# Performance work log

Measured on AMD Instinct MI355X. Metric: run time of the kernel, lower is better.

Reference implementation:

```python
import jax, jax.numpy as jnp
import numpy as np

B, NB, TB = 16, 16, 256          # batch, num cache blocks, tokens per block
EMBED, NH, NKV, HD = 2048, 32, 8, 64  # embed dim, query heads, kv heads, head dim
LAST_OFFSET = 192                # valid length of the final cached block


def setup_inputs() -> dict:
    key = jax.random.key(0)
    ks = jax.random.split(key, 7)
    w = 0.02
    return {
        "x": jax.random.normal(ks[0], (B, 1, EMBED), jnp.float32),
        "blocks_k": jax.random.normal(ks[1], (NB, B, NKV, TB, HD), jnp.float32),
        "blocks_v": jax.random.normal(ks[2], (NB, B, NKV, TB, HD), jnp.float32),
        "Wq": jax.random.normal(ks[3], (EMBED, EMBED), jnp.float32) * w,
        "Wk": jax.random.normal(ks[4], (NKV * HD, EMBED), jnp.float32) * w,
        "Wv": jax.random.normal(ks[5], (NKV * HD, EMBED), jnp.float32) * w,
        "Wo": jax.random.normal(ks[6], (EMBED, EMBED), jnp.float32) * w,
        "last_offset": LAST_OFFSET,
    }


def reference(x, blocks_k, blocks_v, Wq, Wk, Wv, Wo, last_offset):
    # Decode step (T == 1) of GQA MultiHeadAttention with paged/blockwise KV cache.
    Bx, T, C = x.shape                      # T == 1
    nb, _, hkv, tb, hd = blocks_k.shape
    nh = C // hd
    g = nh // hkv                           # GQA group size
    scale = hd ** -0.5

    # Projections (nn.Linear with bias=False => x @ W.T)
    q = (x @ Wq.T).reshape(Bx, hkv, g, hd)          # (B, H_kv, g, D); T==1 folded
    k_cur = (x @ Wk.T).reshape(Bx, hkv, 1, hd)      # (B, H_kv, 1, D)
    v_cur = (x @ Wv.T).reshape(Bx, hkv, 1, hd)

    # Gather cached blocks into a contiguous view: (nb,B,Hkv,tb,D) -> (B,Hkv,nb*tb,D)
    Kc = jnp.transpose(blocks_k, (1, 2, 0, 3, 4)).reshape(Bx, hkv, nb * tb, hd)
    Vc = jnp.transpose(blocks_v, (1, 2, 0, 3, 4)).reshape(Bx, hkv, nb * tb, hd)
    K = jnp.concatenate([Kc, k_cur], axis=2)        # (B, H_kv, nb*tb+1, D)
    V = jnp.concatenate([Vc, v_cur], axis=2)

    # Valid positions: all full blocks, last cached block truncated to last_offset,
    # plus the current token. Equivalent to the streaming softmax over blocks.
    pos = jnp.arange(nb * tb)
    mask = jnp.concatenate([pos < (nb - 1) * tb + last_offset,
                            jnp.ones((1,), dtype=bool)])

    # GQA scores without materializing expanded KV heads
    scores = jnp.einsum('bhgd,bhkd->bhgk', q, K) * scale   # (B, H_kv, g, L)
    scores = jnp.where(mask, scores, jnp.finfo(scores.dtype).min)
    probs = jax.nn.softmax(scores, axis=-1)
    o = jnp.einsum('bhgk,bhkd->bhgd', probs, V)             # (B, H_kv, g, D)

    atten = o.reshape(Bx, 1, C)                              # heads -> channels
    out = atten @ Wo.T                                       # (B, 1, C)
    return out
```

## Files before the change

### kernel.cpp

```cpp
#include <hip/hip_runtime.h>
#include <cstdint>
#include <cstddef>

#define BATCH 16
#define NBLK 16
#define TB 256
#define EMBED 2048
#define NKV 8
#define GQ 4
#define HD 64
#define NQROWS 3072
#define QSCALE 0.18033688011112042f

#define OFF_PARTMS 49152
#define OFF_PARTO  65536
#define OFF_ATTEN  589824

__device__ __forceinline__ float dot4(float4 a, float4 b) {
  return a.x * b.x + a.y * b.y + a.z * b.z + a.w * b.w;
}

template <int CTRL>
__device__ __forceinline__ float dpp_add(float x) {
  return x + __int_as_float(
                 __builtin_amdgcn_mov_dpp(__float_as_int(x), CTRL, 0xF, 0xF, true));
}
__device__ __forceinline__ float red16(float x) {
  x = dpp_add<0xB1>(x);
  x = dpp_add<0x4E>(x);
  x = dpp_add<0x124>(x);
  x = dpp_add<0x128>(x);
  return x;
}

#define PROJ_RPB 4
__global__ __launch_bounds__(256) void proj_kernel(
    const float* __restrict__ x, const float* __restrict__ Wq,
    const float* __restrict__ Wk, const float* __restrict__ Wv,
    float* __restrict__ proj) {
  int tid = threadIdx.x;
  int bb = tid & 15, kc = tid >> 4;
  int row0 = blockIdx.x * PROJ_RPB;
  const float* xp = x + (size_t)bb * EMBED + kc * 128;
  const float* wr[PROJ_RPB];
#pragma unroll
  for (int r = 0; r < PROJ_RPB; ++r) {
    int row = row0 + r;
    wr[r] = (row < 2048 ? Wq + (size_t)row * EMBED
             : row < 2560 ? Wk + (size_t)(row - 2048) * EMBED
                          : Wv + (size_t)(row - 2560) * EMBED) + kc * 128;
  }
  float a[PROJ_RPB] = {0.f, 0.f, 0.f, 0.f};
#pragma unroll
  for (int k = 0; k < 128; k += 8) {
    float4 x0 = *reinterpret_cast<const float4*>(xp + k);
    float4 x1 = *reinterpret_cast<const float4*>(xp + k + 4);
#pragma unroll
    for (int r = 0; r < PROJ_RPB; ++r) {
      float4 w0 = *reinterpret_cast<const float4*>(wr[r] + k);
      float4 w1 = *reinterpret_cast<const float4*>(wr[r] + k + 4);
      a[r] += dot4(w0, x0) + dot4(w1, x1);
    }
  }
  int w = tid >> 6, lane = tid & 63;
  __shared__ float red[4][PROJ_RPB][16];
#pragma unroll
  for (int r = 0; r < PROJ_RPB; ++r) {
    float s = a[r];
    s += __shfl_xor(s, 16);
    s += __shfl_xor(s, 32);
    if (lane < 16) red[w][r][lane] = s;
  }
  __syncthreads();
  if (tid < 16 * PROJ_RPB) {
    int r = tid >> 4, b2 = tid & 15;
    float v = red[0][r][b2] + red[1][r][b2] + red[2][r][b2] + red[3][r][b2];
    proj[(size_t)b2 * NQROWS + row0 + r] = v;
  }
}

template <bool MASKED>
__device__ __forceinline__ void batch16(const float4 qv[GQ], const float4 kv[4],
                                        const float4 vv[4], const bool pr[4],
                                        float m[GQ], float sm[GQ], float4 acc[GQ]) {
  float s[4][GQ];
#pragma unroll
  for (int j = 0; j < 4; ++j)
#pragma unroll
    for (int gi = 0; gi < GQ; ++gi) s[j][gi] = dot4(qv[gi], kv[j]);
#pragma unroll
  for (int j = 0; j < 4; ++j)
#pragma unroll
    for (int gi = 0; gi < GQ; ++gi) {
      s[j][gi] = red16(s[j][gi]);
      if (MASKED && !pr[j]) s[j][gi] = -1e30f;
    }
#pragma unroll
  for (int gi = 0; gi < GQ; ++gi) {
    float bm = fmaxf(fmaxf(s[0][gi], s[1][gi]), fmaxf(s[2][gi], s[3][gi]));
    float mn = fmaxf(m[gi], bm);
    float c = exp2f(m[gi] - mn);
    float p0 = exp2f(s[0][gi] - mn);
    float p1 = exp2f(s[1][gi] - mn);
    float p2 = exp2f(s[2][gi] - mn);
    float p3 = exp2f(s[3][gi] - mn);
    sm[gi] = sm[gi] * c + ((p0 + p1) + (p2 + p3));
    acc[gi].x = acc[gi].x * c + (p0 * vv[0].x + p1 * vv[1].x + p2 * vv[2].x + p3 * vv[3].x);
    acc[gi].y = acc[gi].y * c + (p0 * vv[0].y + p1 * vv[1].y + p2 * vv[2].y + p3 * vv[3].y);
    acc[gi].z = acc[gi].z * c + (p0 * vv[0].z + p1 * vv[1].z + p2 * vv[2].z + p3 * vv[3].z);
    acc[gi].w = acc[gi].w * c + (p0 * vv[0].w + p1 * vv[1].w + p2 * vv[2].w + p3 * vv[3].w);
    m[gi] = mn;
  }
}

__global__ __launch_bounds__(256) void attn_partial_kernel(
    const float* __restrict__ blocks_k, const float* __restrict__ blocks_v,
    const float* __restrict__ proj, const int* __restrict__ last_offset,
    float* __restrict__ part_ms, float* __restrict__ part_o) {
  int nb = blockIdx.x, b = blockIdx.y, h = blockIdx.z;
  int tid = threadIdx.x;
  int w = tid >> 6, lane = tid & 63;
  int sub = lane >> 4, dl = (lane & 15) * 4;

  float4 qv[GQ];
  const float* qbase = proj + (size_t)b * NQROWS + h * GQ * HD + dl;
#pragma unroll
  for (int gi = 0; gi < GQ; ++gi) {
    float4 q = *reinterpret_cast<const float4*>(qbase + gi * HD);
    qv[gi] = make_float4(q.x * QSCALE, q.y * QSCALE, q.z * QSCALE, q.w * QSCALE);
  }

  size_t kvoff = (((size_t)nb * BATCH + b) * NKV + h) * (size_t)(TB * HD);
  const float* kp = blocks_k + kvoff + (size_t)(w * 64 + sub) * HD + dl;
  const float* vp = blocks_v + kvoff + (size_t)(w * 64 + sub) * HD + dl;

  float m[GQ], sm[GQ];
  float4 acc[GQ];
#pragma unroll
  for (int gi = 0; gi < GQ; ++gi) {
    m[gi] = -1e30f;
    sm[gi] = 0.f;
    acc[gi] = make_float4(0.f, 0.f, 0.f, 0.f);
  }

  if (nb != NBLK - 1) {
    bool pr[4] = {true, true, true, true};
#pragma unroll
    for (int ot = 0; ot < 4; ++ot) {
      float4 kv[4], vv[4];
#pragma unroll
      for (int j = 0; j < 4; ++j)
        kv[j] = *reinterpret_cast<const float4*>(kp + (ot * 16 + j * 4) * HD);
#pragma unroll
      for (int j = 0; j < 4; ++j)
        vv[j] = *reinterpret_cast<const float4*>(vp + (ot * 16 + j * 4) * HD);
      batch16<false>(qv, kv, vv, pr, m, sm, acc);
    }
  } else {
    int valid = last_offset[0];
#pragma unroll
    for (int ot = 0; ot < 4; ++ot) {
      float4 kv[4], vv[4];
      bool pr[4];
#pragma unroll
      for (int j = 0; j < 4; ++j) {
        int tok = w * 64 + ot * 16 + j * 4 + sub;
        pr[j] = tok < valid;
        kv[j] = make_float4(0.f, 0.f, 0.f, 0.f);
        vv[j] = make_float4(0.f, 0.f, 0.f, 0.f);
        if (pr[j]) {
          kv[j] = *reinterpret_cast<const float4*>(kp + (ot * 16 + j * 4) * HD);
          vv[j] = *reinterpret_cast<const float4*>(vp + (ot * 16 + j * 4) * HD);
        }
      }
      batch16<true>(qv, kv, vv, pr, m, sm, acc);
    }
  }

#pragma unroll
  for (int mask = 16; mask <= 32; mask <<= 1) {
#pragma unroll
    for (int gi = 0; gi < GQ; ++gi) {
      float mo = __shfl_xor(m[gi], mask);
      float so = __shfl_xor(sm[gi], mask);
      float4 ao;
      ao.x = __shfl_xor(acc[gi].x, mask);
      ao.y = __shfl_xor(acc[gi].y, mask);
      ao.z = __shfl_xor(acc[gi].z, mask);
      ao.w = __shfl_xor(acc[gi].w, mask);
      float mn = fmaxf(m[gi], mo);
      float c1 = exp2f(m[gi] - mn);
      float c2 = exp2f(mo - mn);
      sm[gi] = sm[gi] * c1 + so * c2;
      acc[gi].x = acc[gi].x * c1 + ao.x * c2;
      acc[gi].y = acc[gi].y * c1 + ao.y * c2;
      acc[gi].z = acc[gi].z * c1 + ao.z * c2;
      acc[gi].w = acc[gi].w * c1 + ao.w * c2;
      m[gi] = mn;
    }
  }

  __shared__ float lds_o[4][GQ][HD];
  __shared__ float lds_m[4][GQ];
  __shared__ float lds_s[4][GQ];
  if (lane < 16) {
#pragma unroll
    for (int gi = 0; gi < GQ; ++gi)
      *reinterpret_cast<float4*>(&lds_o[w][gi][dl]) = acc[gi];
    if (lane == 0) {
#pragma unroll
      for (int gi = 0; gi < GQ; ++gi) {
        lds_m[w][gi] = m[gi];
        lds_s[w][gi] = sm[gi];
      }
    }
  }
  __syncthreads();

  if (w == 0) {
    int d = lane;
#pragma unroll
    for (int gi = 0; gi < GQ; ++gi) {
      float M = fmaxf(fmaxf(lds_m[0][gi], lds_m[1][gi]),
                      fmaxf(lds_m[2][gi], lds_m[3][gi]));
      float sum = 0.f, o = 0.f;
#pragma unroll
      for (int ww = 0; ww < 4; ++ww) {
        float c = exp2f(lds_m[ww][gi] - M);
        sum += lds_s[ww][gi] * c;
        o += lds_o[ww][gi][d] * c;
      }
      size_t idx = (((size_t)b * NKV + h) * GQ + gi) * NBLK + nb;
      if (lane == 0) {
        part_ms[idx * 2] = M;
        part_ms[idx * 2 + 1] = sum;
      }
      part_o[idx * HD + d] = o;
    }
  }
}

__global__ __launch_bounds__(256) void reduce_kernel(
    const float* __restrict__ proj, const float* __restrict__ part_ms,
    const float* __restrict__ part_o, float* __restrict__ atten) {
  int tid = threadIdx.x;
  int wi = blockIdx.x * 4 + (tid >> 6);
  int lane = tid & 63;
  int b = wi >> 5;
  int h = (wi >> 2) & 7;
  int gi = wi & 3;
  size_t pidx = (((size_t)b * NKV + h) * GQ + gi) * NBLK;

  float qd = proj[(size_t)b * NQROWS + (h * GQ + gi) * HD + lane];
  float kd = proj[(size_t)b * NQROWS + 2048 + h * HD + lane];
  float vd = proj[(size_t)b * NQROWS + 2560 + h * HD + lane];
  float sp = qd * kd;
#pragma unroll
  for (int mask = 1; mask < 64; mask <<= 1) sp += __shfl_xor(sp, mask);
  float s_cur = sp * QSCALE;

  float pm[NBLK], ps[NBLK];
  float M = s_cur;
#pragma unroll
  for (int nb = 0; nb < NBLK; ++nb) {
    pm[nb] = part_ms[(pidx + nb) * 2];
    ps[nb] = part_ms[(pidx + nb) * 2 + 1];
    M = fmaxf(M, pm[nb]);
  }
  float p_cur = exp2f(s_cur - M);
  float sum = p_cur;
  float o = p_cur * vd;
#pragma unroll
  for (int nb = 0; nb < NBLK; ++nb) {
    float c = exp2f(pm[nb] - M);
    sum += ps[nb] * c;
    o += part_o[(pidx + nb) * HD + lane] * c;
  }
  atten[(size_t)b * EMBED + (h * GQ + gi) * HD + lane] = o / sum;
}

#define OUT_RPB 4
__global__ __launch_bounds__(256) void out_kernel(
    const float* __restrict__ atten, const float* __restrict__ Wo,
    float* __restrict__ out) {
  int tid = threadIdx.x;
  int bb = tid & 15, kc = tid >> 4;
  int row0 = blockIdx.x * OUT_RPB;
  const float* xp = atten + (size_t)bb * EMBED + kc * 128;
  float a[OUT_RPB] = {0.f, 0.f, 0.f, 0.f};
#pragma unroll
  for (int k = 0; k < 128; k += 8) {
    float4 x0 = *reinterpret_cast<const float4*>(xp + k);
    float4 x1 = *reinterpret_cast<const float4*>(xp + k + 4);
#pragma unroll
    for (int r = 0; r < OUT_RPB; ++r) {
      const float* wp = Wo + (size_t)(row0 + r) * EMBED + kc * 128;
      float4 w0 = *reinterpret_cast<const float4*>(wp + k);
      float4 w1 = *reinterpret_cast<const float4*>(wp + k + 4);
      a[r] += dot4(w0, x0) + dot4(w1, x1);
    }
  }
  int w = tid >> 6, lane = tid & 63;
  __shared__ float red[4][OUT_RPB][16];
#pragma unroll
  for (int r = 0; r < OUT_RPB; ++r) {
    float s = a[r];
    s += __shfl_xor(s, 16);
    s += __shfl_xor(s, 32);
    if (lane < 16) red[w][r][lane] = s;
  }
  __syncthreads();
  if (tid < 16 * OUT_RPB) {
    int r = tid >> 4, b2 = tid & 15;
    float v = red[0][r][b2] + red[1][r][b2] + red[2][r][b2] + red[3][r][b2];
    out[(size_t)b2 * EMBED + row0 + r] = v;
  }
}

extern "C" void kernel_launch(void* const* d_in, const int* in_sizes, int n_in,
                              void* d_out, int out_size, void* d_ws, size_t ws_size,
                              hipStream_t stream) {
  const float* x = (const float*)d_in[0];
  const float* bk = (const float*)d_in[1];
  const float* bv = (const float*)d_in[2];
  const float* Wq = (const float*)d_in[3];
  const float* Wk = (const float*)d_in[4];
  const float* Wv = (const float*)d_in[5];
  const float* Wo = (const float*)d_in[6];
  const int* lo = (const int*)d_in[7];

  float* ws = (float*)d_ws;
  float* proj = ws;
  float* part_ms = ws + OFF_PARTMS;
  float* part_o = ws + OFF_PARTO;
  float* atten = ws + OFF_ATTEN;
  float* out = (float*)d_out;

  proj_kernel<<<NQROWS / PROJ_RPB, 256, 0, stream>>>(x, Wq, Wk, Wv, proj);
  attn_partial_kernel<<<dim3(NBLK, BATCH, NKV), 256, 0, stream>>>(
      bk, bv, proj, lo, part_ms, part_o);
  reduce_kernel<<<(BATCH * NKV * GQ) / 4, 256, 0, stream>>>(
      proj, part_ms, part_o, atten);
  out_kernel<<<EMBED / OUT_RPB, 256, 0, stream>>>(atten, Wo, out);
}
```

Before: 122.9 us.

## Stage KV tiles through LDS with async global_load_lds double buffering

The attention partial kernel now copies K and V tiles of 32 tokens into double-buffered shared memory using direct global-to-LDS loads. The next tile is prefetched while the current one is computed, replacing the earlier approach of loading registers directly from global memory. The goal is to overlap memory latency with the softmax/accumulate work. The masked last block now loads all tokens, including invalid ones, and applies the mask per wave group. Each wave covers only 8 rows per tile, so there is less parallelism in flight per load and the work is split into finer-grained steps.

```diff
diff --git a/kernel.cpp b/kernel.cpp
--- a/kernel.cpp
+++ b/kernel.cpp
@@ -12,9 +12,17 @@
 #define NQROWS 3072
 #define QSCALE 0.18033688011112042f
 
+#define TILE_T 32
+#define NTILE 8
+
 #define OFF_PARTMS 49152
 #define OFF_PARTO  65536
 #define OFF_ATTEN  589824
+
+#define GLDS16(gp, lp)                                          \
+  __builtin_amdgcn_global_load_lds(                             \
+      (const __attribute__((address_space(1))) uint32_t*)(gp),  \
+      (__attribute__((address_space(3))) uint32_t*)(lp), 16, 0, 0)
 
 __device__ __forceinline__ float dot4(float4 a, float4 b) {
   return a.x * b.x + a.y * b.y + a.z * b.z + a.w * b.w;
@@ -79,40 +87,6 @@
   }
 }
 
-template <bool MASKED>
-__device__ __forceinline__ void batch16(const float4 qv[GQ], const float4 kv[4],
-                                        const float4 vv[4], const bool pr[4],
-                                        float m[GQ], float sm[GQ], float4 acc[GQ]) {
-  float s[4][GQ];
-#pragma unroll
-  for (int j = 0; j < 4; ++j)
-#pragma unroll
-    for (int gi = 0; gi < GQ; ++gi) s[j][gi] = dot4(qv[gi], kv[j]);
-#pragma unroll
-  for (int j = 0; j < 4; ++j)
-#pragma unroll
-    for (int gi = 0; gi < GQ; ++gi) {
-      s[j][gi] = red16(s[j][gi]);
-      if (MASKED && !pr[j]) s[j][gi] = -1e30f;
-    }
-#pragma unroll
-  for (int gi = 0; gi < GQ; ++gi) {
-    float bm = fmaxf(fmaxf(s[0][gi], s[1][gi]), fmaxf(s[2][gi], s[3][gi]));
-    float mn = fmaxf(m[gi], bm);
-    float c = exp2f(m[gi] - mn);
-    float p0 = exp2f(s[0][gi] - mn);
-    float p1 = exp2f(s[1][gi] - mn);
-    float p2 = exp2f(s[2][gi] - mn);
-    float p3 = exp2f(s[3][gi] - mn);
-    sm[gi] = sm[gi] * c + ((p0 + p1) + (p2 + p3));
-    acc[gi].x = acc[gi].x * c + (p0 * vv[0].x + p1 * vv[1].x + p2 * vv[2].x + p3 * vv[3].x);
-    acc[gi].y = acc[gi].y * c + (p0 * vv[0].y + p1 * vv[1].y + p2 * vv[2].y + p3 * vv[3].y);
-    acc[gi].z = acc[gi].z * c + (p0 * vv[0].z + p1 * vv[1].z + p2 * vv[2].z + p3 * vv[3].z);
-    acc[gi].w = acc[gi].w * c + (p0 * vv[0].w + p1 * vv[1].w + p2 * vv[2].w + p3 * vv[3].w);
-    m[gi] = mn;
-  }
-}
-
 __global__ __launch_bounds__(256) void attn_partial_kernel(
     const float* __restrict__ blocks_k, const float* __restrict__ blocks_v,
     const float* __restrict__ proj, const int* __restrict__ last_offset,
@@ -121,6 +95,12 @@
   int tid = threadIdx.x;
   int w = tid >> 6, lane = tid & 63;
   int sub = lane >> 4, dl = (lane & 15) * 4;
+  int myrow = w * 8;
+
+  __shared__ __align__(16) float lds_k[2][TILE_T * HD];
+  __shared__ __align__(16) float lds_v[2][TILE_T * HD];
+
+  int valid = (nb == NBLK - 1) ? last_offset[0] : TB;
 
   float4 qv[GQ];
   const float* qbase = proj + (size_t)b * NQROWS + h * GQ * HD + dl;
@@ -129,10 +109,11 @@
     float4 q = *reinterpret_cast<const float4*>(qbase + gi * HD);
     qv[gi] = make_float4(q.x * QSCALE, q.y * QSCALE, q.z * QSCALE, q.w * QSCALE);
   }
+  asm volatile("s_waitcnt vmcnt(0)" ::: "memory");
 
   size_t kvoff = (((size_t)nb * BATCH + b) * NKV + h) * (size_t)(TB * HD);
-  const float* kp = blocks_k + kvoff + (size_t)(w * 64 + sub) * HD + dl;
-  const float* vp = blocks_v + kvoff + (size_t)(w * 64 + sub) * HD + dl;
+  const float* kg = blocks_k + kvoff;
+  const float* vg = blocks_v + kvoff;
 
   float m[GQ], sm[GQ];
   float4 acc[GQ];
@@ -143,38 +124,69 @@
     acc[gi] = make_float4(0.f, 0.f, 0.f, 0.f);
   }
 
-  if (nb != NBLK - 1) {
-    bool pr[4] = {true, true, true, true};
-#pragma unroll
-    for (int ot = 0; ot < 4; ++ot) {
-      float4 kv[4], vv[4];
-#pragma unroll
-      for (int j = 0; j < 4; ++j)
-        kv[j] = *reinterpret_cast<const float4*>(kp + (ot * 16 + j * 4) * HD);
-#pragma unroll
-      for (int j = 0; j < 4; ++j)
-        vv[j] = *reinterpret_cast<const float4*>(vp + (ot * 16 + j * 4) * HD);
-      batch16<false>(qv, kv, vv, pr, m, sm, acc);
-    }
-  } else {
-    int valid = last_offset[0];
-#pragma unroll
-    for (int ot = 0; ot < 4; ++ot) {
-      float4 kv[4], vv[4];
-      bool pr[4];
-#pragma unroll
-      for (int j = 0; j < 4; ++j) {
-        int tok = w * 64 + ot * 16 + j * 4 + sub;
-        pr[j] = tok < valid;
-        kv[j] = make_float4(0.f, 0.f, 0.f, 0.f);
-        vv[j] = make_float4(0.f, 0.f, 0.f, 0.f);
-        if (pr[j]) {
-          kv[j] = *reinterpret_cast<const float4*>(kp + (ot * 16 + j * 4) * HD);
-          vv[j] = *reinterpret_cast<const float4*>(vp + (ot * 16 + j * 4) * HD);
-        }
-      }
-      batch16<true>(qv, kv, vv, pr, m, sm, acc);
-    }
+  auto STAGE = [&](int it, int buf) {
+    int gbase = (it * TILE_T + myrow) * HD + lane * 4;
+#pragma unroll
+    for (int i = 0; i < 2; ++i) {
+      GLDS16(kg + gbase + i * 4 * HD, &lds_k[buf][(myrow + i * 4) * HD]);
+      GLDS16(vg + gbase + i * 4 * HD, &lds_v[buf][(myrow + i * 4) * HD]);
+    }
+  };
+
+  auto COMPUTE = [&](int it, int buf, bool masked) {
+    float4 kf[2], vf[2];
+#pragma unroll
+    for (int grp = 0; grp < 2; ++grp) {
+      kf[grp] = *reinterpret_cast<const float4*>(
+          &lds_k[buf][(myrow + grp * 4 + sub) * HD + dl]);
+      vf[grp] = *reinterpret_cast<const float4*>(
+          &lds_v[buf][(myrow + grp * 4 + sub) * HD + dl]);
+    }
+    float s[2][GQ];
+#pragma unroll
+    for (int grp = 0; grp < 2; ++grp)
+#pragma unroll
+      for (int gi = 0; gi < GQ; ++gi) s[grp][gi] = dot4(qv[gi], kf[grp]);
+#pragma unroll
+    for (int grp = 0; grp < 2; ++grp)
+#pragma unroll
+      for (int gi = 0; gi < GQ; ++gi) s[grp][gi] = red16(s[grp][gi]);
+    if (masked) {
+      int tok0 = it * TILE_T + myrow + sub;
+#pragma unroll
+      for (int grp = 0; grp < 2; ++grp)
+        if (tok0 + grp * 4 >= valid)
+#pragma unroll
+          for (int gi = 0; gi < GQ; ++gi) s[grp][gi] = -1e30f;
+    }
+#pragma unroll
+    for (int gi = 0; gi < GQ; ++gi) {
+      float bm = fmaxf(s[0][gi], s[1][gi]);
+      float mn = fmaxf(m[gi], bm);
+      float c = exp2f(m[gi] - mn);
+      float p0 = exp2f(s[0][gi] - mn);
+      float p1 = exp2f(s[1][gi] - mn);
+      sm[gi] = sm[gi] * c + (p0 + p1);
+      acc[gi].x = acc[gi].x * c + (p0 * vf[0].x + p1 * vf[1].x);
+      acc[gi].y = acc[gi].y * c + (p0 * vf[0].y + p1 * vf[1].y);
+      acc[gi].z = acc[gi].z * c + (p0 * vf[0].z + p1 * vf[1].z);
+      acc[gi].w = acc[gi].w * c + (p0 * vf[0].w + p1 * vf[1].w);
+      m[gi] = mn;
+    }
+  };
+
+  STAGE(0, 0);
+#pragma unroll
+  for (int it = 0; it < NTILE; ++it) {
+    if (it + 1 < NTILE) {
+      STAGE(it + 1, (it + 1) & 1);
+      asm volatile("s_waitcnt vmcnt(4)" ::: "memory");
+    } else {
+      asm volatile("s_waitcnt vmcnt(0)" ::: "memory");
+    }
+    __builtin_amdgcn_sched_barrier(0);
+    bool masked = (it * TILE_T + myrow + 8) > valid;
+    COMPUTE(it, it & 1, masked);
   }
 
 #pragma unroll
```

Result: slower. 128.0 us (+4.2%).

## Split fused flash-decode attention into separate score, softmax, and PV kernels

Applied to the files above, without the earlier changes.

Replaces the single online-softmax partial attention kernel with three passes: a score kernel writing Q·K scores to a workspace buffer, a softmax kernel computing the global max, sum and probabilities per (batch, head, group), and a PV kernel that accumulates probability-weighted V without rescaling. This removes the per-tile running max/exp rescaling and the max/sum merge logic in the reduction. In exchange it adds two kernel launches and round-trips roughly 8 MB of scores plus 8 MB of probabilities through global memory, and the softmax pass runs on only 128 blocks. It also no longer skips the masked tail of the last block, so those K/V loads now happen.

```diff
diff --git a/kernel.cpp b/kernel.cpp
--- a/kernel.cpp
+++ b/kernel.cpp
@@ -10,11 +10,15 @@
 #define GQ 4
 #define HD 64
 #define NQROWS 3072
+#define TTOT 4096
 #define QSCALE 0.18033688011112042f
 
-#define OFF_PARTMS 49152
-#define OFF_PARTO  65536
-#define OFF_ATTEN  589824
+#define OFF_SUMS   49152
+#define OFF_PCUR   49664
+#define OFF_PARTO  50176
+#define OFF_ATTEN  574464
+#define OFF_S      607232
+#define OFF_P      2704384
 
 __device__ __forceinline__ float dot4(float4 a, float4 b) {
   return a.x * b.x + a.y * b.y + a.z * b.z + a.w * b.w;
@@ -24,13 +28,6 @@
 __device__ __forceinline__ float dpp_add(float x) {
   return x + __int_as_float(
                  __builtin_amdgcn_mov_dpp(__float_as_int(x), CTRL, 0xF, 0xF, true));
-}
-__device__ __forceinline__ float red16(float x) {
-  x = dpp_add<0xB1>(x);
-  x = dpp_add<0x4E>(x);
-  x = dpp_add<0x124>(x);
-  x = dpp_add<0x128>(x);
-  return x;
 }
 
 #define PROJ_RPB 4
@@ -79,204 +76,171 @@
   }
 }
 
-template <bool MASKED>
-__device__ __forceinline__ void batch16(const float4 qv[GQ], const float4 kv[4],
-                                        const float4 vv[4], const bool pr[4],
-                                        float m[GQ], float sm[GQ], float4 acc[GQ]) {
-  float s[4][GQ];
-#pragma unroll
-  for (int j = 0; j < 4; ++j)
-#pragma unroll
-    for (int gi = 0; gi < GQ; ++gi) s[j][gi] = dot4(qv[gi], kv[j]);
-#pragma unroll
-  for (int j = 0; j < 4; ++j)
+__global__ __launch_bounds__(256) void score_kernel(
+    const float* __restrict__ blocks_k, const float* __restrict__ proj,
+    float* __restrict__ sbuf) {
+  int nb = blockIdx.x, b = blockIdx.y, h = blockIdx.z;
+  int tid = threadIdx.x;
+  int w = tid >> 6, lane = tid & 63;
+  int tq = lane >> 2;
+  int qd = lane & 3;
+
+  float4 qv[GQ][4];
+  const float* qbase = proj + (size_t)b * NQROWS + h * GQ * HD + qd * 16;
+#pragma unroll
+  for (int gi = 0; gi < GQ; ++gi)
+#pragma unroll
+    for (int j = 0; j < 4; ++j)
+      qv[gi][j] = *reinterpret_cast<const float4*>(qbase + gi * HD + j * 4);
+
+  const float* kg = blocks_k + (((size_t)nb * BATCH + b) * NKV + h) * (TB * HD);
+  float* sout = sbuf + ((size_t)(b * NKV + h)) * (TTOT * GQ) +
+                (size_t)(nb * TB + w * 64) * GQ;
+
+#pragma unroll
+  for (int i = 0; i < 4; ++i) {
+    int tl = w * 64 + i * 16 + tq;
+    const float* kp = kg + (size_t)tl * HD + qd * 16;
+    float4 k0 = *reinterpret_cast<const float4*>(kp);
+    float4 k1 = *reinterpret_cast<const float4*>(kp + 4);
+    float4 k2 = *reinterpret_cast<const float4*>(kp + 8);
+    float4 k3 = *reinterpret_cast<const float4*>(kp + 12);
+    float s[GQ];
 #pragma unroll
     for (int gi = 0; gi < GQ; ++gi) {
-      s[j][gi] = red16(s[j][gi]);
-      if (MASKED && !pr[j]) s[j][gi] = -1e30f;
-    }
-#pragma unroll
-  for (int gi = 0; gi < GQ; ++gi) {
-    float bm = fmaxf(fmaxf(s[0][gi], s[1][gi]), fmaxf(s[2][gi], s[3][gi]));
-    float mn = fmaxf(m[gi], bm);
-    float c = exp2f(m[gi] - mn);
-    float p0 = exp2f(s[0][gi] - mn);
-    float p1 = exp2f(s[1][gi] - mn);
-    float p2 = exp2f(s[2][gi] - mn);
-    float p3 = exp2f(s[3][gi] - mn);
-    sm[gi] = sm[gi] * c + ((p0 + p1) + (p2 + p3));
-    acc[gi].x = acc[gi].x * c + (p0 * vv[0].x + p1 * vv[1].x + p2 * vv[2].x + p3 * vv[3].x);
-    acc[gi].y = acc[gi].y * c + (p0 * vv[0].y + p1 * vv[1].y + p2 * vv[2].y + p3 * vv[3].y);
-    acc[gi].z = acc[gi].z * c + (p0 * vv[0].z + p1 * vv[1].z + p2 * vv[2].z + p3 * vv[3].z);
-    acc[gi].w = acc[gi].w * c + (p0 * vv[0].w + p1 * vv[1].w + p2 * vv[2].w + p3 * vv[3].w);
-    m[gi] = mn;
-  }
-}
-
-__global__ __launch_bounds__(256) void attn_partial_kernel(
-    const float* __restrict__ blocks_k, const float* __restrict__ blocks_v,
-    const float* __restrict__ proj, const int* __restrict__ last_offset,
-    float* __restrict__ part_ms, float* __restrict__ part_o) {
+      s[gi] = dot4(qv[gi][0], k0) + dot4(qv[gi][1], k1) +
+              dot4(qv[gi][2], k2) + dot4(qv[gi][3], k3);
+      s[gi] = dpp_add<0xB1>(s[gi]);
+      s[gi] = dpp_add<0x4E>(s[gi]);
+    }
+    float v01 = (qd & 1) ? s[1] : s[0];
+    float v23 = (qd & 1) ? s[3] : s[2];
+    float v = (qd & 2) ? v23 : v01;
+    sout[(size_t)(i * 16) * GQ + lane] = v;
+  }
+}
+
+__global__ __launch_bounds__(256) void softmax_kernel(
+    const float* __restrict__ sbuf, const float* __restrict__ proj,
+    const int* __restrict__ last_offset, float* __restrict__ pbuf,
+    float* __restrict__ sums, float* __restrict__ pcur) {
+  int bh = blockIdx.x;
+  int b = bh >> 3, h = bh & 7;
+  int gi = threadIdx.x >> 6, lane = threadIdx.x & 63;
+  int valid = (NBLK - 1) * TB + last_offset[0];
+
+  const float* srow = sbuf + (size_t)bh * (TTOT * GQ);
+  float* prow = pbuf + ((size_t)bh * GQ + gi) * TTOT;
+
+  float qd = proj[(size_t)b * NQROWS + (h * GQ + gi) * HD + lane];
+  float kd = proj[(size_t)b * NQROWS + 2048 + h * HD + lane];
+  float sp = qd * kd;
+#pragma unroll
+  for (int mask = 1; mask < 64; mask <<= 1) sp += __shfl_xor(sp, mask);
+  float s_cur = sp;
+
+  float mx = s_cur;
+#pragma unroll 8
+  for (int i = 0; i < TTOT / 64; ++i) {
+    int t = i * 64 + lane;
+    float v = srow[(size_t)t * GQ + gi];
+    if (t < valid) mx = fmaxf(mx, v);
+  }
+#pragma unroll
+  for (int mask = 1; mask < 64; mask <<= 1) mx = fmaxf(mx, __shfl_xor(mx, mask));
+
+  float sum = 0.f;
+#pragma unroll 8
+  for (int i = 0; i < TTOT / 64; ++i) {
+    int t = i * 64 + lane;
+    float v = srow[(size_t)t * GQ + gi];
+    float p = (t < valid) ? exp2f((v - mx) * QSCALE) : 0.f;
+    sum += p;
+    prow[t] = p;
+  }
+#pragma unroll
+  for (int mask = 1; mask < 64; mask <<= 1) sum += __shfl_xor(sum, mask);
+  float p_c = exp2f((s_cur - mx) * QSCALE);
+  if (lane == 0) {
+    sums[bh * GQ + gi] = sum + p_c;
+    pcur[bh * GQ + gi] = p_c;
+  }
+}
+
+__global__ __launch_bounds__(256) void pv_kernel(
+    const float* __restrict__ blocks_v, const float* __restrict__ pbuf,
+    float* __restrict__ part_o) {
   int nb = blockIdx.x, b = blockIdx.y, h = blockIdx.z;
   int tid = threadIdx.x;
   int w = tid >> 6, lane = tid & 63;
   int sub = lane >> 4, dl = (lane & 15) * 4;
 
-  float4 qv[GQ];
-  const float* qbase = proj + (size_t)b * NQROWS + h * GQ * HD + dl;
-#pragma unroll
-  for (int gi = 0; gi < GQ; ++gi) {
-    float4 q = *reinterpret_cast<const float4*>(qbase + gi * HD);
-    qv[gi] = make_float4(q.x * QSCALE, q.y * QSCALE, q.z * QSCALE, q.w * QSCALE);
-  }
-
-  size_t kvoff = (((size_t)nb * BATCH + b) * NKV + h) * (size_t)(TB * HD);
-  const float* kp = blocks_k + kvoff + (size_t)(w * 64 + sub) * HD + dl;
-  const float* vp = blocks_v + kvoff + (size_t)(w * 64 + sub) * HD + dl;
-
-  float m[GQ], sm[GQ];
+  const float* vg = blocks_v + (((size_t)nb * BATCH + b) * NKV + h) * (TB * HD);
+  const float* pg = pbuf + ((size_t)(b * NKV + h)) * (GQ * TTOT) + nb * TB;
+
   float4 acc[GQ];
 #pragma unroll
-  for (int gi = 0; gi < GQ; ++gi) {
-    m[gi] = -1e30f;
-    sm[gi] = 0.f;
-    acc[gi] = make_float4(0.f, 0.f, 0.f, 0.f);
-  }
-
-  if (nb != NBLK - 1) {
-    bool pr[4] = {true, true, true, true};
-#pragma unroll
-    for (int ot = 0; ot < 4; ++ot) {
-      float4 kv[4], vv[4];
-#pragma unroll
-      for (int j = 0; j < 4; ++j)
-        kv[j] = *reinterpret_cast<const float4*>(kp + (ot * 16 + j * 4) * HD);
-#pragma unroll
-      for (int j = 0; j < 4; ++j)
-        vv[j] = *reinterpret_cast<const float4*>(vp + (ot * 16 + j * 4) * HD);
-      batch16<false>(qv, kv, vv, pr, m, sm, acc);
-    }
-  } else {
-    int valid = last_offset[0];
-#pragma unroll
-    for (int ot = 0; ot < 4; ++ot) {
-      float4 kv[4], vv[4];
-      bool pr[4];
-#pragma unroll
-      for (int j = 0; j < 4; ++j) {
-        int tok = w * 64 + ot * 16 + j * 4 + sub;
-        pr[j] = tok < valid;
-        kv[j] = make_float4(0.f, 0.f, 0.f, 0.f);
-        vv[j] = make_float4(0.f, 0.f, 0.f, 0.f);
-        if (pr[j]) {
-          kv[j] = *reinterpret_cast<const float4*>(kp + (ot * 16 + j * 4) * HD);
-          vv[j] = *reinterpret_cast<const float4*>(vp + (ot * 16 + j * 4) * HD);
-        }
-      }
-      batch16<true>(qv, kv, vv, pr, m, sm, acc);
-    }
+  for (int gi = 0; gi < GQ; ++gi) acc[gi] = make_float4(0.f, 0.f, 0.f, 0.f);
+
+#pragma unroll
+  for (int i = 0; i < 16; ++i) {
+    int tl = w * 64 + i * 4 + sub;
+    float4 v4 = *reinterpret_cast<const float4*>(vg + (size_t)tl * HD + dl);
+    float p0 = pg[0 * TTOT + tl];
+    float p1 = pg[1 * TTOT + tl];
+    float p2 = pg[2 * TTOT + tl];
+    float p3 = pg[3 * TTOT + tl];
+    acc[0].x += p0 * v4.x; acc[0].y += p0 * v4.y; acc[0].z += p0 * v4.z; acc[0].w += p0 * v4.w;
+    acc[1].x += p1 * v4.x; acc[1].y += p1 * v4.y; acc[1].z += p1 * v4.z; acc[1].w += p1 * v4.w;
+    acc[2].x += p2 * v4.x; acc[2].y += p2 * v4.y; acc[2].z += p2 * v4.z; acc[2].w += p2 * v4.w;
+    acc[3].x += p3 * v4.x; acc[3].y += p3 * v4.y; acc[3].z += p3 * v4.z; acc[3].w += p3 * v4.w;
   }
 
 #pragma unroll
   for (int mask = 16; mask <= 32; mask <<= 1) {
 #pragma unroll
     for (int gi = 0; gi < GQ; ++gi) {
-      float mo = __shfl_xor(m[gi], mask);
-      float so = __shfl_xor(sm[gi], mask);
-      float4 ao;
-      ao.x = __shfl_xor(acc[gi].x, mask);
-      ao.y = __shfl_xor(acc[gi].y, mask);
-      ao.z = __shfl_xor(acc[gi].z, mask);
-      ao.w = __shfl_xor(acc[gi].w, mask);
-      float mn = fmaxf(m[gi], mo);
-      float c1 = exp2f(m[gi] - mn);
-      float c2 = exp2f(mo - mn);
-      sm[gi] = sm[gi] * c1 + so * c2;
-      acc[gi].x = acc[gi].x * c1 + ao.x * c2;
-      acc[gi].y = acc[gi].y * c1 + ao.y * c2;
-      acc[gi].z = acc[gi].z * c1 + ao.z * c2;
-      acc[gi].w = acc[gi].w * c1 + ao.w * c2;
-      m[gi] = mn;
+      acc[gi].x += __shfl_xor(acc[gi].x, mask);
+      acc[gi].y += __shfl_xor(acc[gi].y, mask);
+      acc[gi].z += __shfl_xor(acc[gi].z, mask);
+      acc[gi].w += __shfl_xor(acc[gi].w, mask);
     }
   }
 
   __shared__ float lds_o[4][GQ][HD];
-  __shared__ float lds_m[4][GQ];
-  __shared__ float lds_s[4][GQ];
   if (lane < 16) {
 #pragma unroll
     for (int gi = 0; gi < GQ; ++gi)
       *reinterpret_cast<float4*>(&lds_o[w][gi][dl]) = acc[gi];
-    if (lane == 0) {
-#pragma unroll
-      for (int gi = 0; gi < GQ; ++gi) {
-        lds_m[w][gi] = m[gi];
-        lds_s[w][gi] = sm[gi];
-      }
-    }
   }
   __syncthreads();
-
   if (w == 0) {
     int d = lane;
 #pragma unroll
     for (int gi = 0; gi < GQ; ++gi) {
-      float M = fmaxf(fmaxf(lds_m[0][gi], lds_m[1][gi]),
-                      fmaxf(lds_m[2][gi], lds_m[3][gi]));
-      float sum = 0.f, o = 0.f;
-#pragma unroll
-      for (int ww = 0; ww < 4; ++ww) {
-        float c = exp2f(lds_m[ww][gi] - M);
-        sum += lds_s[ww][gi] * c;
-        o += lds_o[ww][gi][d] * c;
-      }
-      size_t idx = (((size_t)b * NKV + h) * GQ + gi) * NBLK + nb;
-      if (lane == 0) {
-        part_ms[idx * 2] = M;
-        part_ms[idx * 2 + 1] = sum;
-      }
-      part_o[idx * HD + d] = o;
+      float o = lds_o[0][gi][d] + lds_o[1][gi][d] + lds_o[2][gi][d] + lds_o[3][gi][d];
+      part_o[(((size_t)(b * NKV + h) * GQ + gi) * NBLK + nb) * HD + d] = o;
     }
   }
 }
 
 __global__ __launch_bounds__(256) void reduce_kernel(
-    const float* __restrict__ proj, const float* __restrict__ part_ms,
-    const float* __restrict__ part_o, float* __restrict__ atten) {
+    const float* __restrict__ proj, const float* __restrict__ part_o,
+    const float* __restrict__ sums, const float* __restrict__ pcur,
+    float* __restrict__ atten) {
   int tid = threadIdx.x;
   int wi = blockIdx.x * 4 + (tid >> 6);
   int lane = tid & 63;
   int b = wi >> 5;
   int h = (wi >> 2) & 7;
   int gi = wi & 3;
-  size_t pidx = (((size_t)b * NKV + h) * GQ + gi) * NBLK;
-
-  float qd = proj[(size_t)b * NQROWS + (h * GQ + gi) * HD + lane];
-  float kd = proj[(size_t)b * NQROWS + 2048 + h * HD + lane];
+  size_t pidx = ((size_t)(b * NKV + h) * GQ + gi) * NBLK;
+
   float vd = proj[(size_t)b * NQROWS + 2560 + h * HD + lane];
-  float sp = qd * kd;
-#pragma unroll
-  for (int mask = 1; mask < 64; mask <<= 1) sp += __shfl_xor(sp, mask);
-  float s_cur = sp * QSCALE;
-
-  float pm[NBLK], ps[NBLK];
-  float M = s_cur;
-#pragma unroll
-  for (int nb = 0; nb < NBLK; ++nb) {
-    pm[nb] = part_ms[(pidx + nb) * 2];
-    ps[nb] = part_ms[(pidx + nb) * 2 + 1];
-    M = fmaxf(M, pm[nb]);
-  }
-  float p_cur = exp2f(s_cur - M);
-  float sum = p_cur;
-  float o = p_cur * vd;
-#pragma unroll
-  for (int nb = 0; nb < NBLK; ++nb) {
-    float c = exp2f(pm[nb] - M);
-    sum += ps[nb] * c;
-    o += part_o[(pidx + nb) * HD + lane] * c;
-  }
-  atten[(size_t)b * EMBED + (h * GQ + gi) * HD + lane] = o / sum;
+  float o = pcur[wi] * vd;
+#pragma unroll
+  for (int nb = 0; nb < NBLK; ++nb) o += part_o[(pidx + nb) * HD + lane];
+  atten[(size_t)b * EMBED + (h * GQ + gi) * HD + lane] = o / sums[wi];
 }
 
 #define OUT_RPB 4
@@ -331,15 +295,19 @@
 
   float* ws = (float*)d_ws;
   float* proj = ws;
-  float* part_ms = ws + OFF_PARTMS;
+  float* sums = ws + OFF_SUMS;
+  float* pcur = ws + OFF_PCUR;
   float* part_o = ws + OFF_PARTO;
   float* atten = ws + OFF_ATTEN;
+  float* sbuf = ws + OFF_S;
+  float* pbuf = ws + OFF_P;
   float* out = (float*)d_out;
 
   proj_kernel<<<NQROWS / PROJ_RPB, 256, 0, stream>>>(x, Wq, Wk, Wv, proj);
-  attn_partial_kernel<<<dim3(NBLK, BATCH, NKV), 256, 0, stream>>>(
-      bk, bv, proj, lo, part_ms, part_o);
-  reduce_kernel<<<(BATCH * NKV * GQ) / 4, 256, 0, stream>>>(
-      proj, part_ms, part_o, atten);
+  score_kernel<<<dim3(NBLK, BATCH, NKV), 256, 0, stream>>>(bk, proj, sbuf);
+  softmax_kernel<<<BATCH * NKV, 256, 0, stream>>>(sbuf, proj, lo, pbuf, sums, pcur);
+  pv_kernel<<<dim3(NBLK, BATCH, NKV), 256, 0, stream>>>(bv, pbuf, part_o);
+  reduce_kernel<<<(BATCH * NKV * GQ) / 4, 256, 0, stream>>>(proj, part_o, sums,
+                                                            pcur, atten);
   out_kernel<<<EMBED / OUT_RPB, 256, 0, stream>>>(atten, Wo, out);
 }
```

Result: slower. 165.3 us (+34.5%).

## Double-buffer KV loads with inline-asm nontemporal bursts and explicit vmcnt waits

Applied to the files above, without the earlier changes.

Replaces the per-iteration compiler-scheduled K/V loads in the attention partial kernel with hand-written global_load_dwordx4 bursts using the nt hint. Two register buffers alternate so the next 16-token tile is in flight while the current one is computed, with s_waitcnt vmcnt(8) gating each step. The masked and unmasked paths are merged into one predicate-driven path, so the last block now loads all tokens and masks them afterwards instead of skipping the loads. This adds register pressure and relies on manual wait counts that the compiler cannot check.

```diff
diff --git a/kernel.cpp b/kernel.cpp
--- a/kernel.cpp
+++ b/kernel.cpp
@@ -16,9 +16,36 @@
 #define OFF_PARTO  65536
 #define OFF_ATTEN  589824
 
+typedef float f32x4 __attribute__((ext_vector_type(4)));
+
 __device__ __forceinline__ float dot4(float4 a, float4 b) {
   return a.x * b.x + a.y * b.y + a.z * b.z + a.w * b.w;
 }
+__device__ __forceinline__ float dot4x(float4 a, f32x4 b) {
+  return a.x * b.x + a.y * b.y + a.z * b.z + a.w * b.w;
+}
+
+__device__ __forceinline__ void burst8(const float* kp, const float* vp,
+                                       f32x4& k0, f32x4& k1, f32x4& k2, f32x4& k3,
+                                       f32x4& v0, f32x4& v1, f32x4& v2, f32x4& v3) {
+  asm volatile(
+      "global_load_dwordx4 %0, %8, off nt\n\t"
+      "global_load_dwordx4 %1, %8, off offset:1024 nt\n\t"
+      "global_load_dwordx4 %2, %8, off offset:2048 nt\n\t"
+      "global_load_dwordx4 %3, %8, off offset:3072 nt\n\t"
+      "global_load_dwordx4 %4, %9, off nt\n\t"
+      "global_load_dwordx4 %5, %9, off offset:1024 nt\n\t"
+      "global_load_dwordx4 %6, %9, off offset:2048 nt\n\t"
+      "global_load_dwordx4 %7, %9, off offset:3072 nt"
+      : "=v"(k0), "=v"(k1), "=v"(k2), "=v"(k3),
+        "=v"(v0), "=v"(v1), "=v"(v2), "=v"(v3)
+      : "v"(kp), "v"(vp));
+}
+
+#define WAIT8 do { asm volatile("s_waitcnt vmcnt(8)" ::: "memory"); \
+                   __builtin_amdgcn_sched_barrier(0); } while (0)
+#define WAIT0 do { asm volatile("s_waitcnt vmcnt(0)" ::: "memory"); \
+                   __builtin_amdgcn_sched_barrier(0); } while (0)
 
 template <int CTRL>
 __device__ __forceinline__ float dpp_add(float x) {
@@ -79,21 +106,20 @@
   }
 }
 
-template <bool MASKED>
-__device__ __forceinline__ void batch16(const float4 qv[GQ], const float4 kv[4],
-                                        const float4 vv[4], const bool pr[4],
-                                        float m[GQ], float sm[GQ], float4 acc[GQ]) {
+__device__ __forceinline__ void batch16m(const float4 qv[GQ], const f32x4 kv[4],
+                                         const f32x4 vv[4], const bool pr[4],
+                                         float m[GQ], float sm[GQ], float4 acc[GQ]) {
   float s[4][GQ];
 #pragma unroll
   for (int j = 0; j < 4; ++j)
 #pragma unroll
-    for (int gi = 0; gi < GQ; ++gi) s[j][gi] = dot4(qv[gi], kv[j]);
+    for (int gi = 0; gi < GQ; ++gi) s[j][gi] = dot4x(qv[gi], kv[j]);
 #pragma unroll
   for (int j = 0; j < 4; ++j)
 #pragma unroll
     for (int gi = 0; gi < GQ; ++gi) {
       s[j][gi] = red16(s[j][gi]);
-      if (MASKED && !pr[j]) s[j][gi] = -1e30f;
+      if (!pr[j]) s[j][gi] = -1e30f;
     }
 #pragma unroll
   for (int gi = 0; gi < GQ; ++gi) {
@@ -122,6 +148,8 @@
   int w = tid >> 6, lane = tid & 63;
   int sub = lane >> 4, dl = (lane & 15) * 4;
 
+  int valid = (nb == NBLK - 1) ? last_offset[0] : TB;
+
   float4 qv[GQ];
   const float* qbase = proj + (size_t)b * NQROWS + h * GQ * HD + dl;
 #pragma unroll
@@ -133,6 +161,13 @@
   size_t kvoff = (((size_t)nb * BATCH + b) * NKV + h) * (size_t)(TB * HD);
   const float* kp = blocks_k + kvoff + (size_t)(w * 64 + sub) * HD + dl;
   const float* vp = blocks_v + kvoff + (size_t)(w * 64 + sub) * HD + dl;
+
+  bool pr[4][4];
+#pragma unroll
+  for (int ot = 0; ot < 4; ++ot)
+#pragma unroll
+    for (int j = 0; j < 4; ++j)
+      pr[ot][j] = (w * 64 + ot * 16 + j * 4 + sub) < valid;
 
   float m[GQ], sm[GQ];
   float4 acc[GQ];
@@ -143,39 +178,24 @@
     acc[gi] = make_float4(0.f, 0.f, 0.f, 0.f);
   }
 
-  if (nb != NBLK - 1) {
-    bool pr[4] = {true, true, true, true};
-#pragma unroll
-    for (int ot = 0; ot < 4; ++ot) {
-      float4 kv[4], vv[4];
-#pragma unroll
-      for (int j = 0; j < 4; ++j)
-        kv[j] = *reinterpret_cast<const float4*>(kp + (ot * 16 + j * 4) * HD);
-#pragma unroll
-      for (int j = 0; j < 4; ++j)
-        vv[j] = *reinterpret_cast<const float4*>(vp + (ot * 16 + j * 4) * HD);
-      batch16<false>(qv, kv, vv, pr, m, sm, acc);
-    }
-  } else {
-    int valid = last_offset[0];
-#pragma unroll
-    for (int ot = 0; ot < 4; ++ot) {
-      float4 kv[4], vv[4];
-      bool pr[4];
-#pragma unroll
-      for (int j = 0; j < 4; ++j) {
-        int tok = w * 64 + ot * 16 + j * 4 + sub;
-        pr[j] = tok < valid;
-        kv[j] = make_float4(0.f, 0.f, 0.f, 0.f);
-        vv[j] = make_float4(0.f, 0.f, 0.f, 0.f);
-        if (pr[j]) {
-          kv[j] = *reinterpret_cast<const float4*>(kp + (ot * 16 + j * 4) * HD);
-          vv[j] = *reinterpret_cast<const float4*>(vp + (ot * 16 + j * 4) * HD);
-        }
-      }
-      batch16<true>(qv, kv, vv, pr, m, sm, acc);
-    }
-  }
+  asm volatile("s_waitcnt vmcnt(0)" ::: "memory");
+
+  f32x4 ka[4], va[4], kb[4], vb[4];
+  burst8(kp, vp, ka[0], ka[1], ka[2], ka[3], va[0], va[1], va[2], va[3]);
+  burst8(kp + 16 * HD, vp + 16 * HD, kb[0], kb[1], kb[2], kb[3],
+         vb[0], vb[1], vb[2], vb[3]);
+  WAIT8;
+  batch16m(qv, ka, va, pr[0], m, sm, acc);
+  burst8(kp + 32 * HD, vp + 32 * HD, ka[0], ka[1], ka[2], ka[3],
+         va[0], va[1], va[2], va[3]);
+  WAIT8;
+  batch16m(qv, kb, vb, pr[1], m, sm, acc);
+  burst8(kp + 48 * HD, vp + 48 * HD, kb[0], kb[1], kb[2], kb[3],
+         vb[0], vb[1], vb[2], vb[3]);
+  WAIT8;
+  batch16m(qv, ka, va, pr[2], m, sm, acc);
+  WAIT0;
+  batch16m(qv, kb, vb, pr[3], m, sm, acc);
 
 #pragma unroll
   for (int mask = 16; mask <= 32; mask <<= 1) {
```

New measurement: 141.4 us. 15.0% more time.
